# Kernel tuning notes

Measured on AMD Instinct MI355X. Metric: run time of the kernel, lower is better.

## Reference

```python
import jax, jax.numpy as jnp
import numpy as np

N_NODES = 50000


def _gine(x, src, dst, edge_embed, lin_w, lin_b, nn_w, nn_b):
    # PyG GINEConv (eps=0): out = nn(x + sum_{j->i} ReLU(x_j + lin(edge_attr)))
    e = edge_embed @ lin_w + lin_b              # [E, d_in]
    msg = jax.nn.relu(x[src] + e)               # gather + fuse, [E, d_in]
    agg = jax.ops.segment_sum(msg, dst, num_segments=N_NODES)  # scatter-add, [N, d_in]
    return (x + agg) @ nn_w + nn_b              # small MLP, [N, d_out]


def setup_inputs() -> dict:
    key = jax.random.key(0)
    ks = jax.random.split(key, 20)
    E = 800000
    h = 128
    sc = lambda f_in: 1.0 / np.sqrt(f_in)
    inp = {
        "x": jax.random.normal(ks[0], (N_NODES, 1), jnp.float32),
        "edge_index": jax.random.randint(ks[1], (2, E), 0, N_NODES, jnp.int64),
        "edge_attr": jax.random.normal(ks[2], (E, 1), jnp.float32),
        "em_w": jax.random.normal(ks[3], (1, h), jnp.float32) * sc(1),
        "em_b": jnp.zeros((h,), jnp.float32),
        "l1_w": jax.random.normal(ks[4], (h, 1), jnp.float32) * sc(h),
        "l1_b": jnp.zeros((1,), jnp.float32),
        "n1_w": jax.random.normal(ks[5], (1, h), jnp.float32) * sc(1),
        "n1_b": jnp.zeros((h,), jnp.float32),
        "l2_w": jax.random.normal(ks[6], (h, h), jnp.float32) * sc(h),
        "l2_b": jnp.zeros((h,), jnp.float32),
        "n2_w": jax.random.normal(ks[7], (h, h), jnp.float32) * sc(h),
        "n2_b": jnp.zeros((h,), jnp.float32),
        "l3_w": jax.random.normal(ks[8], (h, h), jnp.float32) * sc(h),
        "l3_b": jnp.zeros((h,), jnp.float32),
        "n3_w": jax.random.normal(ks[9], (h, h), jnp.float32) * sc(h),
        "n3_b": jnp.zeros((h,), jnp.float32),
        "dec_w": jax.random.normal(ks[10], (2 * h, 1), jnp.float32) * sc(2 * h),
        "dec_b": jnp.zeros((1,), jnp.float32),
    }
    return inp


def reference(x, edge_index, edge_attr, em_w, em_b, l1_w, l1_b, n1_w, n1_b,
              l2_w, l2_b, n2_w, n2_b, l3_w, l3_b, n3_w, n3_b, dec_w, dec_b):
    src, dst = edge_index[0], edge_index[1]
    edge_embed = edge_attr @ em_w + em_b                      # [E, 128]
    hdn = _gine(x,   src, dst, edge_embed, l1_w, l1_b, n1_w, n1_b)
    hdn = _gine(hdn, src, dst, edge_embed, l2_w, l2_b, n2_w, n2_b)
    hdn = _gine(hdn, src, dst, edge_embed, l3_w, l3_b, n3_w, n3_b)
    h_cat = jnp.concatenate([hdn[src], hdn[dst]], axis=-1)    # [E, 256]
    return h_cat @ dec_w + dec_b                              # [E, 1]
```

## Files before the change

kernel.cpp:

```cpp
#include <hip/hip_runtime.h>

#define H 128
#define CAPC 3072


typedef unsigned long long ull;
using bf16x8 = __attribute__((ext_vector_type(8))) short;
using f32x4  = __attribute__((ext_vector_type(4))) float;

__device__ __forceinline__ float bf2f(unsigned short v) {
  return __uint_as_float(((unsigned)v) << 16);
}
__device__ __forceinline__ unsigned short bf16r(float v) {
  unsigned u = __float_as_uint(v);
  u = (u + 0x7FFFu + ((u >> 16) & 1u)) >> 16;
  return (unsigned short)u;
}
__device__ __forceinline__ unsigned bf16pair(float a, float b) {
  return (unsigned)bf16r(a) | ((unsigned)bf16r(b) << 16);
}

__global__ __launch_bounds__(256) void init_consts(
    const float* __restrict__ em_w, const float* __restrict__ em_b,
    const float* __restrict__ l1_w, const float* __restrict__ l1_b,
    const float* __restrict__ l2_w, const float* __restrict__ l2_b,
    const float* __restrict__ n1_b,
    const float* __restrict__ l3_w, const float* __restrict__ l3_b,
    const float* __restrict__ n2w, const float* __restrict__ n3w,
    float* __restrict__ consts, int* __restrict__ cursor,
    unsigned short* __restrict__ w2t, unsigned short* __restrict__ w3t) {
  if (blockIdx.x > 0) {
    const int i = (blockIdx.x - 1) * 256 + threadIdx.x;
    if (i < H * H) {
      const int j = i >> 7, k = i & (H - 1);
      w2t[k * H + j] = bf16r(n2w[i]);
    } else {
      const int ii = i - H * H;
      const int j = ii >> 7, k = ii & (H - 1);
      w3t[k * H + j] = bf16r(n3w[ii]);
    }
    return;
  }
  const int k = threadIdx.x;
  cursor[k] = 0;
  cursor[k + 256] = 0;
  __shared__ float sa[H], sc[H];
  if (k < H) {
    float u2 = 0.f, c2 = 0.f, u3 = 0.f, c3 = 0.f;
    for (int j = 0; j < H; ++j) {
      const float ew = em_w[j], eb = em_b[j];
      u2 = fmaf(ew, l2_w[j * H + k], u2);
      c2 = fmaf(eb, l2_w[j * H + k], c2);
      u3 = fmaf(ew, l3_w[j * H + k], u3);
      c3 = fmaf(eb, l3_w[j * H + k], c3);
    }
    consts[2 + k]         = u2;
    consts[2 + H + k]     = c2 + l2_b[k] + n1_b[k];
    consts[2 + 2 * H + k] = u3;
    consts[2 + 3 * H + k] = c3 + l3_b[k];
    sa[k] = em_w[k] * l1_w[k];
    sc[k] = em_b[k] * l1_w[k];
  }
  __syncthreads();
  for (int s = 64; s > 0; s >>= 1) {
    if (k < s) { sa[k] += sa[k + s]; sc[k] += sc[k + s]; }
    __syncthreads();
  }
  if (k == 0) { consts[0] = sa[0]; consts[1] = sc[0] + l1_b[0]; }
}

__global__ __launch_bounds__(1024) void bin_scatter(
    const int* __restrict__ src, const int* __restrict__ dst,
    const float* __restrict__ ea, int* __restrict__ cursor,
    ull* __restrict__ spc, int E, int NBUCK) {
  __shared__ int lhist[512];
  __shared__ int lbase[512];
  const int tid = threadIdx.x;
  const int base = blockIdx.x * 2048 + tid * 2;
  if (tid < 512) lhist[tid] = 0;
  __syncthreads();
  int s_[2], d_[2], b_[2], r_[2];
  float a_[2];
#pragma unroll
  for (int j = 0; j < 2; ++j) {
    const int e = base + j;
    if (e < E) {
      s_[j] = src[e]; d_[j] = dst[e]; a_[j] = ea[e];
      b_[j] = d_[j] >> 7;
      r_[j] = atomicAdd(&lhist[b_[j]], 1);
    } else {
      b_[j] = -1;
    }
  }
  __syncthreads();
  if (tid < NBUCK && lhist[tid] > 0)
    lbase[tid] = atomicAdd(&cursor[tid], lhist[tid]);
  __syncthreads();
#pragma unroll
  for (int j = 0; j < 2; ++j) {
    if (b_[j] >= 0) {
      const int pl = lbase[b_[j]] + r_[j];
      if (pl < CAPC)
        spc[(size_t)b_[j] * CAPC + pl] =
            ((ull)(unsigned)(s_[j] | ((d_[j] & 127) << 16)) << 32) |
            (ull)(unsigned)__float_as_uint(a_[j]);
    }
  }
}

__global__ __launch_bounds__(1024) void fine_scatter(
    const int* __restrict__ cursor, const ull* __restrict__ spc,
    const float* __restrict__ x, const float* __restrict__ consts,
    int2* __restrict__ spf, int* __restrict__ rowstart,
    float* __restrict__ s1, int N) {
  __shared__ int lh[128];
  __shared__ int sd[128];
  __shared__ int cur[128];
  __shared__ int2 pay[CAPC];
  const int tid = threadIdx.x;
  const int b = blockIdx.x;
  const int cnt = min(cursor[b], CAPC);
  const size_t rbase = (size_t)b * CAPC;
  if (tid < 128) lh[tid] = 0;
  __syncthreads();
  for (int i = tid; i < cnt; i += 1024)
    atomicAdd(&lh[(int)((spc[rbase + i] >> 48) & 127u)], 1);
  __syncthreads();
  if (tid < 128) sd[tid] = lh[tid];
  __syncthreads();
  for (int off = 1; off < 128; off <<= 1) {
    int t = 0;
    if (tid < 128 && tid >= off) t = sd[tid - off];
    __syncthreads();
    if (tid < 128) sd[tid] += t;
    __syncthreads();
  }
  if (tid < 128) {
    const int ex = sd[tid] - lh[tid];
    cur[tid] = ex;
    rowstart[b * 129 + tid] = (int)rbase + ex;
    if (tid == 0) rowstart[b * 129 + 128] = (int)rbase + cnt;
  }
  __syncthreads();
  for (int i = tid; i < cnt; i += 1024) {
    const ull payv = spc[rbase + i];
    const int dl = (int)((payv >> 48) & 127u);
    const int pos = atomicAdd(&cur[dl], 1);
    pay[pos] = make_int2((int)((payv >> 32) & 0xFFFFu), (int)(unsigned)payv);
  }
  __syncthreads();
  for (int i = tid; i < cnt; i += 1024) spf[rbase + i] = pay[i];
  const int lane = tid & 63, w = tid >> 6;
  const float a1 = consts[0], c1 = consts[1];
  for (int i = w; i < 128; i += 16) {
    const int n = (b << 7) + i;
    if (n >= N) break;
    const int rsl = sd[i] - lh[i], ci = lh[i];
    float part = 0.f;
    for (int j = lane; j < ci; j += 64) {
      const int2 pv = pay[rsl + j];
      part += fmaxf(x[pv.x] + fmaf(a1, __int_as_float(pv.y), c1), 0.f);
    }
#pragma unroll
    for (int o = 32; o >= 1; o >>= 1) part += __shfl_xor(part, o, 64);
    if (lane == 0) s1[n] = x[n] + part;
  }
}

__global__ __launch_bounds__(1024) void layer2_fused(
    const int* __restrict__ rowstart, const int2* __restrict__ sp,
    const float* __restrict__ s1, const float* __restrict__ n1w,
    const float* __restrict__ n1b, const float* __restrict__ consts,
    const unsigned short* __restrict__ w2t, const float* __restrict__ n2b,
    unsigned short* __restrict__ h2b, int N) {
  __shared__ unsigned short t2s[16][136];
  __shared__ unsigned short hs[16][128];
  const int tid = threadIdx.x, w = tid >> 6, lane = tid & 63;
  const int node0 = blockIdx.x * 16;
  {
    const int n = node0 + w;
    if (n < N) {
      const int rb = (n >> 7) * 129 + (n & 127);
      const int rs = rowstart[rb], re = rowstart[rb + 1];
      const float w0 = n1w[lane],            w1 = n1w[lane + 64];
      const float u0 = consts[2 + lane],     u1 = consts[2 + lane + 64];
      const float c0 = consts[2 + H + lane], c1 = consts[2 + H + lane + 64];
      float acc0 = 0.f, acc1 = 0.f;
      for (int base = rs; base < re; base += 64) {
        const int i = base + lane;
        float s1v = 0.f, eav = 0.f;
        if (i < re) {
          const int2 sv = sp[i];
          s1v = s1[sv.x];
          eav = __int_as_float(sv.y);
        }
        const int cntv = min(64, re - base);
        for (int j = 0; j < cntv; ++j) {
          const float s = __shfl(s1v, j, 64);
          const float a = __shfl(eav, j, 64);
          acc0 += fmaxf(fmaf(s, w0, fmaf(a, u0, c0)), 0.f);
          acc1 += fmaxf(fmaf(s, w1, fmaf(a, u1, c1)), 0.f);
        }
      }
      const float sn = s1[n];
      t2s[w][lane]      = bf16r(fmaf(sn, w0, n1b[lane])      + acc0);
      t2s[w][lane + 64] = bf16r(fmaf(sn, w1, n1b[lane + 64]) + acc1);
    } else {
      t2s[w][lane] = 0;
      t2s[w][lane + 64] = 0;
    }
  }
  __syncthreads();
  if (w < 8) {
    const int t = w, col = lane & 15, quad = lane >> 4;
    const bf16x8 a0 = *(const bf16x8*)&t2s[col][quad * 8];
    const bf16x8 a1 = *(const bf16x8*)&t2s[col][32 + quad * 8];
    const bf16x8 a2 = *(const bf16x8*)&t2s[col][64 + quad * 8];
    const bf16x8 a3 = *(const bf16x8*)&t2s[col][96 + quad * 8];
    const bf16x8* bcol =
        (const bf16x8*)(w2t + (size_t)(t * 16 + col) * H + quad * 8);
    f32x4 acc = {0.f, 0.f, 0.f, 0.f};
    acc = __builtin_amdgcn_mfma_f32_16x16x32_bf16(a0, bcol[0], acc, 0, 0, 0);
    acc = __builtin_amdgcn_mfma_f32_16x16x32_bf16(a1, bcol[4], acc, 0, 0, 0);
    acc = __builtin_amdgcn_mfma_f32_16x16x32_bf16(a2, bcol[8], acc, 0, 0, 0);
    acc = __builtin_amdgcn_mfma_f32_16x16x32_bf16(a3, bcol[12], acc, 0, 0, 0);
    const float bias = n2b[t * 16 + col];
#pragma unroll
    for (int r = 0; r < 4; ++r)
      hs[quad * 4 + r][t * 16 + col] = bf16r(acc[r] + bias);
  }
  __syncthreads();
  const int row = tid >> 6, word = tid & 63;
  ((unsigned*)h2b)[(size_t)(node0 + row) * 64 + word] =
      ((const unsigned*)hs)[row * 64 + word];
}

__global__ __launch_bounds__(1024) void layer3_fused(
    const int* __restrict__ rowstart, const int2* __restrict__ sp,
    const unsigned short* __restrict__ h2b, const float* __restrict__ consts,
    const unsigned short* __restrict__ w3t, const float* __restrict__ n3b,
    const float* __restrict__ dec_w, float* __restrict__ p,
    float* __restrict__ q, int N) {
  __shared__ unsigned short t3s[16][136];
  __shared__ float ps[16], qs[16];
  const int tid = threadIdx.x, w = tid >> 6, lane = tid & 63;
  const int node0 = blockIdx.x * 16;
  if (tid < 16) { ps[tid] = 0.f; qs[tid] = 0.f; }
  {
    const int n = node0 + w;
    const int k0 = 2 * lane;
    if (n < N) {
      const int rb = (n >> 7) * 129 + (n & 127);
      const int rs = rowstart[rb], re = rowstart[rb + 1];
      const float u0 = consts[2 + 2 * H + k0], u1 = consts[2 + 2 * H + k0 + 1];
      const float c0 = consts[2 + 3 * H + k0], c1 = consts[2 + 3 * H + k0 + 1];
      float acc0 = 0.f, acc1 = 0.f;
      for (int base = rs; base < re; base += 64) {
        const int i = base + lane;
        int esrc = 0;
        float eav = 0.f;
        if (i < re) {
          const int2 sv = sp[i];
          esrc = sv.x;
          eav = __int_as_float(sv.y);
        }
        const int cntv = min(64, re - base);
        int j = 0;
        for (; j + 4 <= cntv; j += 4) {
          const int s0 = __shfl(esrc, j, 64),     s1i = __shfl(esrc, j + 1, 64);
          const int s2 = __shfl(esrc, j + 2, 64), s3 = __shfl(esrc, j + 3, 64);
          const float a0 = __shfl(eav, j, 64),     a1 = __shfl(eav, j + 1, 64);
          const float a2 = __shfl(eav, j + 2, 64), a3 = __shfl(eav, j + 3, 64);
          const ushort2 h0 = *(const ushort2*)&h2b[(size_t)s0 * H + k0];
          const ushort2 h1 = *(const ushort2*)&h2b[(size_t)s1i * H + k0];
          const ushort2 h2v = *(const ushort2*)&h2b[(size_t)s2 * H + k0];
          const ushort2 h3 = *(const ushort2*)&h2b[(size_t)s3 * H + k0];
          acc0 += fmaxf(bf2f(h0.x) + fmaf(a0, u0, c0), 0.f);
          acc1 += fmaxf(bf2f(h0.y) + fmaf(a0, u1, c1), 0.f);
          acc0 += fmaxf(bf2f(h1.x) + fmaf(a1, u0, c0), 0.f);
          acc1 += fmaxf(bf2f(h1.y) + fmaf(a1, u1, c1), 0.f);
          acc0 += fmaxf(bf2f(h2v.x) + fmaf(a2, u0, c0), 0.f);
          acc1 += fmaxf(bf2f(h2v.y) + fmaf(a2, u1, c1), 0.f);
          acc0 += fmaxf(bf2f(h3.x) + fmaf(a3, u0, c0), 0.f);
          acc1 += fmaxf(bf2f(h3.y) + fmaf(a3, u1, c1), 0.f);
        }
        for (; j < cntv; ++j) {
          const int s0 = __shfl(esrc, j, 64);
          const float a0 = __shfl(eav, j, 64);
          const ushort2 hv = *(const ushort2*)&h2b[(size_t)s0 * H + k0];
          acc0 += fmaxf(bf2f(hv.x) + fmaf(a0, u0, c0), 0.f);
          acc1 += fmaxf(bf2f(hv.y) + fmaf(a0, u1, c1), 0.f);
        }
      }
      const ushort2 hn = *(const ushort2*)&h2b[(size_t)n * H + k0];
      *(unsigned*)&t3s[w][k0] = bf16pair(bf2f(hn.x) + acc0, bf2f(hn.y) + acc1);
    } else {
      *(unsigned*)&t3s[w][k0] = 0u;
    }
  }
  __syncthreads();
  if (w < 8) {
    const int t = w, col = lane & 15, quad = lane >> 4;
    const bf16x8 a0 = *(const bf16x8*)&t3s[col][quad * 8];
    const bf16x8 a1 = *(const bf16x8*)&t3s[col][32 + quad * 8];
    const bf16x8 a2 = *(const bf16x8*)&t3s[col][64 + quad * 8];
    const bf16x8 a3 = *(const bf16x8*)&t3s[col][96 + quad * 8];
    const bf16x8* bcol =
        (const bf16x8*)(w3t + (size_t)(t * 16 + col) * H + quad * 8);
    f32x4 acc = {0.f, 0.f, 0.f, 0.f};
    acc = __builtin_amdgcn_mfma_f32_16x16x32_bf16(a0, bcol[0], acc, 0, 0, 0);
    acc = __builtin_amdgcn_mfma_f32_16x16x32_bf16(a1, bcol[4], acc, 0, 0, 0);
    acc = __builtin_amdgcn_mfma_f32_16x16x32_bf16(a2, bcol[8], acc, 0, 0, 0);
    acc = __builtin_amdgcn_mfma_f32_16x16x32_bf16(a3, bcol[12], acc, 0, 0, 0);
    const float bias = n3b[t * 16 + col];
    const float dA = dec_w[t * 16 + col];
    const float dB = dec_w[128 + t * 16 + col];
    float pP[4], qP[4];
#pragma unroll
    for (int r = 0; r < 4; ++r) {
      const float h = acc[r] + bias;
      pP[r] = h * dA;
      qP[r] = h * dB;
    }
#pragma unroll
    for (int o = 1; o < 16; o <<= 1) {
#pragma unroll
      for (int r = 0; r < 4; ++r) {
        pP[r] += __shfl_xor(pP[r], o, 64);
        qP[r] += __shfl_xor(qP[r], o, 64);
      }
    }
    if (col == 0) {
#pragma unroll
      for (int r = 0; r < 4; ++r) {
        atomicAdd(&ps[quad * 4 + r], pP[r]);
        atomicAdd(&qs[quad * 4 + r], qP[r]);
      }
    }
  }
  __syncthreads();
  if (tid < 16) {
    const int n = node0 + tid;
    if (n < N) { p[n] = ps[tid]; q[n] = qs[tid]; }
  }
}

__global__ void final_kernel(const int* __restrict__ src,
                             const int* __restrict__ dst,
                             const float* __restrict__ p,
                             const float* __restrict__ q,
                             const float* __restrict__ dec_b,
                             float* __restrict__ out, int E) {
  const int e = blockIdx.x * blockDim.x + threadIdx.x;
  if (e < E) out[e] = p[src[e]] + q[dst[e]] + dec_b[0];
}

extern "C" void kernel_launch(void* const* d_in, const int* in_sizes, int n_in,
                              void* d_out, int out_size, void* d_ws, size_t ws_size,
                              hipStream_t stream) {
  const float* x     = (const float*)d_in[0];
  const int*   ei    = (const int*)d_in[1];
  const float* ea    = (const float*)d_in[2];
  const float* em_w  = (const float*)d_in[3];
  const float* em_b  = (const float*)d_in[4];
  const float* l1_w  = (const float*)d_in[5];
  const float* l1_b  = (const float*)d_in[6];
  const float* n1_w  = (const float*)d_in[7];
  const float* n1_b  = (const float*)d_in[8];
  const float* l2_w  = (const float*)d_in[9];
  const float* l2_b  = (const float*)d_in[10];
  const float* n2_w  = (const float*)d_in[11];
  const float* n2_b  = (const float*)d_in[12];
  const float* l3_w  = (const float*)d_in[13];
  const float* l3_b  = (const float*)d_in[14];
  const float* n3_w  = (const float*)d_in[15];
  const float* n3_b  = (const float*)d_in[16];
  const float* dec_w = (const float*)d_in[17];
  const float* dec_b = (const float*)d_in[18];
  float* out = (float*)d_out;

  const int N = in_sizes[0];
  const int E = in_sizes[2];
  const int* src = ei;
  const int* dst = ei + E;

  const int NBUCK  = (N + 127) >> 7;
  const int NBATCH = (E + 2047) >> 11;
  const int NPAD   = ((N + 15) / 16) * 16;
  const int NT16   = NPAD / 16;

  float* ws       = (float*)d_ws;
  float* consts   = ws;
  ull*   spc      = (ull*)(ws + 1024);
  int2*  spf      = (int2*)(spc + (size_t)NBUCK * CAPC);
  unsigned short* h2b = (unsigned short*)(spf + (size_t)NBUCK * CAPC);
  unsigned short* w2t = h2b + (size_t)NPAD * H;
  unsigned short* w3t = w2t + H * H;
  float* s1       = (float*)(w3t + H * H);
  float* p        = s1 + N;
  float* q        = p + N;
  int*   cursor   = (int*)(q + N);
  int*   rowstart = cursor + 512;

  init_consts<<<129, 256, 0, stream>>>(em_w, em_b, l1_w, l1_b, l2_w, l2_b,
                                       n1_b, l3_w, l3_b, n2_w, n3_w,
                                       consts, cursor, w2t, w3t);
  bin_scatter<<<NBATCH, 1024, 0, stream>>>(src, dst, ea, cursor, spc, E, NBUCK);
  fine_scatter<<<NBUCK, 1024, 0, stream>>>(cursor, spc, x, consts, spf,
                                           rowstart, s1, N);
  layer2_fused<<<NT16, 1024, 0, stream>>>(rowstart, spf, s1, n1_w, n1_b,
                                          consts, w2t, n2_b, h2b, N);
  layer3_fused<<<NT16, 1024, 0, stream>>>(rowstart, spf, h2b, consts, w3t,
                                          n3_b, dec_w, p, q, N);
  final_kernel<<<(E + 255) / 256, 256, 0, stream>>>(src, dst, p, q, dec_b, out, E);
}
```

Before: 230.9 us.

## Fold layer-3 MLP into decoder vectors, replacing MFMA with per-node dot products

Because layer 3's output feeds only the linear decoder, the change precomputes n3_w·dec_w halves (vA, vB) and the bias terms in init_consts. Layer 3 then reduces each node's aggregated feature vector to two scalars p and q with a wave dot product. This drops the MFMA GEMM, the shared-memory staging, the block syncs and the w3t transpose. Layer 3 now runs as 256-thread blocks with one wave per node. Numerics change slightly because the aggregate stays in fp32 instead of being rounded to bf16 before the GEMM.

Result: faster. 219.4 us (median of 2 runs) (-5.0%).

```diff
diff --git a/kernel.cpp b/kernel.cpp
--- a/kernel.cpp
+++ b/kernel.cpp
@@ -27,17 +27,14 @@
     const float* __restrict__ n1_b,
     const float* __restrict__ l3_w, const float* __restrict__ l3_b,
     const float* __restrict__ n2w, const float* __restrict__ n3w,
+    const float* __restrict__ n3b, const float* __restrict__ dec_w,
     float* __restrict__ consts, int* __restrict__ cursor,
-    unsigned short* __restrict__ w2t, unsigned short* __restrict__ w3t) {
+    unsigned short* __restrict__ w2t) {
   if (blockIdx.x > 0) {
     const int i = (blockIdx.x - 1) * 256 + threadIdx.x;
     if (i < H * H) {
       const int j = i >> 7, k = i & (H - 1);
       w2t[k * H + j] = bf16r(n2w[i]);
-    } else {
-      const int ii = i - H * H;
-      const int j = ii >> 7, k = ii & (H - 1);
-      w3t[k * H + j] = bf16r(n3w[ii]);
     }
     return;
   }
@@ -46,18 +43,22 @@
   cursor[k + 256] = 0;
   __shared__ float sa[H], sc[H];
   if (k < H) {
-    float u2 = 0.f, c2 = 0.f, u3 = 0.f, c3 = 0.f;
+    float u2 = 0.f, c2 = 0.f, u3 = 0.f, c3 = 0.f, vA = 0.f, vB = 0.f;
     for (int j = 0; j < H; ++j) {
       const float ew = em_w[j], eb = em_b[j];
       u2 = fmaf(ew, l2_w[j * H + k], u2);
       c2 = fmaf(eb, l2_w[j * H + k], c2);
       u3 = fmaf(ew, l3_w[j * H + k], u3);
       c3 = fmaf(eb, l3_w[j * H + k], c3);
+      vA = fmaf(n3w[k * H + j], dec_w[j], vA);
+      vB = fmaf(n3w[k * H + j], dec_w[H + j], vB);
     }
     consts[2 + k]         = u2;
     consts[2 + H + k]     = c2 + l2_b[k] + n1_b[k];
     consts[2 + 2 * H + k] = u3;
     consts[2 + 3 * H + k] = c3 + l3_b[k];
+    consts[514 + k]       = vA;
+    consts[642 + k]       = vB;
     sa[k] = em_w[k] * l1_w[k];
     sc[k] = em_b[k] * l1_w[k];
   }
@@ -67,6 +68,17 @@
     __syncthreads();
   }
   if (k == 0) { consts[0] = sa[0]; consts[1] = sc[0] + l1_b[0]; }
+  __syncthreads();
+  if (k < H) {
+    sa[k] = n3b[k] * dec_w[k];
+    sc[k] = n3b[k] * dec_w[H + k];
+  }
+  __syncthreads();
+  for (int s = 64; s > 0; s >>= 1) {
+    if (k < s) { sa[k] += sa[k + s]; sc[k] += sc[k + s]; }
+    __syncthreads();
+  }
+  if (k == 0) { consts[770] = sa[0]; consts[771] = sc[0]; }
 }
 
 __global__ __launch_bounds__(1024) void bin_scatter(
@@ -235,113 +247,71 @@
       ((const unsigned*)hs)[row * 64 + word];
 }
 
-__global__ __launch_bounds__(1024) void layer3_fused(
+__global__ __launch_bounds__(256) void layer3_dot(
     const int* __restrict__ rowstart, const int2* __restrict__ sp,
     const unsigned short* __restrict__ h2b, const float* __restrict__ consts,
-    const unsigned short* __restrict__ w3t, const float* __restrict__ n3b,
-    const float* __restrict__ dec_w, float* __restrict__ p,
-    float* __restrict__ q, int N) {
-  __shared__ unsigned short t3s[16][136];
-  __shared__ float ps[16], qs[16];
-  const int tid = threadIdx.x, w = tid >> 6, lane = tid & 63;
-  const int node0 = blockIdx.x * 16;
-  if (tid < 16) { ps[tid] = 0.f; qs[tid] = 0.f; }
-  {
-    const int n = node0 + w;
-    const int k0 = 2 * lane;
-    if (n < N) {
-      const int rb = (n >> 7) * 129 + (n & 127);
-      const int rs = rowstart[rb], re = rowstart[rb + 1];
-      const float u0 = consts[2 + 2 * H + k0], u1 = consts[2 + 2 * H + k0 + 1];
-      const float c0 = consts[2 + 3 * H + k0], c1 = consts[2 + 3 * H + k0 + 1];
-      float acc0 = 0.f, acc1 = 0.f;
-      for (int base = rs; base < re; base += 64) {
-        const int i = base + lane;
-        int esrc = 0;
-        float eav = 0.f;
-        if (i < re) {
-          const int2 sv = sp[i];
-          esrc = sv.x;
-          eav = __int_as_float(sv.y);
-        }
-        const int cntv = min(64, re - base);
-        int j = 0;
-        for (; j + 4 <= cntv; j += 4) {
-          const int s0 = __shfl(esrc, j, 64),     s1i = __shfl(esrc, j + 1, 64);
-          const int s2 = __shfl(esrc, j + 2, 64), s3 = __shfl(esrc, j + 3, 64);
-          const float a0 = __shfl(eav, j, 64),     a1 = __shfl(eav, j + 1, 64);
-          const float a2 = __shfl(eav, j + 2, 64), a3 = __shfl(eav, j + 3, 64);
-          const ushort2 h0 = *(const ushort2*)&h2b[(size_t)s0 * H + k0];
-          const ushort2 h1 = *(const ushort2*)&h2b[(size_t)s1i * H + k0];
-          const ushort2 h2v = *(const ushort2*)&h2b[(size_t)s2 * H + k0];
-          const ushort2 h3 = *(const ushort2*)&h2b[(size_t)s3 * H + k0];
-          acc0 += fmaxf(bf2f(h0.x) + fmaf(a0, u0, c0), 0.f);
-          acc1 += fmaxf(bf2f(h0.y) + fmaf(a0, u1, c1), 0.f);
-          acc0 += fmaxf(bf2f(h1.x) + fmaf(a1, u0, c0), 0.f);
-          acc1 += fmaxf(bf2f(h1.y) + fmaf(a1, u1, c1), 0.f);
-          acc0 += fmaxf(bf2f(h2v.x) + fmaf(a2, u0, c0), 0.f);
-          acc1 += fmaxf(bf2f(h2v.y) + fmaf(a2, u1, c1), 0.f);
-          acc0 += fmaxf(bf2f(h3.x) + fmaf(a3, u0, c0), 0.f);
-          acc1 += fmaxf(bf2f(h3.y) + fmaf(a3, u1, c1), 0.f);
-        }
-        for (; j < cntv; ++j) {
-          const int s0 = __shfl(esrc, j, 64);
-          const float a0 = __shfl(eav, j, 64);
-          const ushort2 hv = *(const ushort2*)&h2b[(size_t)s0 * H + k0];
-          acc0 += fmaxf(bf2f(hv.x) + fmaf(a0, u0, c0), 0.f);
-          acc1 += fmaxf(bf2f(hv.y) + fmaf(a0, u1, c1), 0.f);
-        }
-      }
-      const ushort2 hn = *(const ushort2*)&h2b[(size_t)n * H + k0];
-      *(unsigned*)&t3s[w][k0] = bf16pair(bf2f(hn.x) + acc0, bf2f(hn.y) + acc1);
-    } else {
-      *(unsigned*)&t3s[w][k0] = 0u;
-    }
-  }
-  __syncthreads();
-  if (w < 8) {
-    const int t = w, col = lane & 15, quad = lane >> 4;
-    const bf16x8 a0 = *(const bf16x8*)&t3s[col][quad * 8];
-    const bf16x8 a1 = *(const bf16x8*)&t3s[col][32 + quad * 8];
-    const bf16x8 a2 = *(const bf16x8*)&t3s[col][64 + quad * 8];
-    const bf16x8 a3 = *(const bf16x8*)&t3s[col][96 + quad * 8];
-    const bf16x8* bcol =
-        (const bf16x8*)(w3t + (size_t)(t * 16 + col) * H + quad * 8);
-    f32x4 acc = {0.f, 0.f, 0.f, 0.f};
-    acc = __builtin_amdgcn_mfma_f32_16x16x32_bf16(a0, bcol[0], acc, 0, 0, 0);
-    acc = __builtin_amdgcn_mfma_f32_16x16x32_bf16(a1, bcol[4], acc, 0, 0, 0);
-    acc = __builtin_amdgcn_mfma_f32_16x16x32_bf16(a2, bcol[8], acc, 0, 0, 0);
-    acc = __builtin_amdgcn_mfma_f32_16x16x32_bf16(a3, bcol[12], acc, 0, 0, 0);
-    const float bias = n3b[t * 16 + col];
-    const float dA = dec_w[t * 16 + col];
-    const float dB = dec_w[128 + t * 16 + col];
-    float pP[4], qP[4];
-#pragma unroll
-    for (int r = 0; r < 4; ++r) {
-      const float h = acc[r] + bias;
-      pP[r] = h * dA;
-      qP[r] = h * dB;
-    }
-#pragma unroll
-    for (int o = 1; o < 16; o <<= 1) {
-#pragma unroll
-      for (int r = 0; r < 4; ++r) {
-        pP[r] += __shfl_xor(pP[r], o, 64);
-        qP[r] += __shfl_xor(qP[r], o, 64);
-      }
-    }
-    if (col == 0) {
-#pragma unroll
-      for (int r = 0; r < 4; ++r) {
-        atomicAdd(&ps[quad * 4 + r], pP[r]);
-        atomicAdd(&qs[quad * 4 + r], qP[r]);
-      }
-    }
-  }
-  __syncthreads();
-  if (tid < 16) {
-    const int n = node0 + tid;
-    if (n < N) { p[n] = ps[tid]; q[n] = qs[tid]; }
+    float* __restrict__ p, float* __restrict__ q, int N) {
+  const int n = (blockIdx.x * blockDim.x + threadIdx.x) >> 6;
+  const int lane = threadIdx.x & 63;
+  if (n >= N) return;
+  const int k0 = 2 * lane;
+  const float u0 = consts[2 + 2 * H + k0], u1 = consts[2 + 2 * H + k0 + 1];
+  const float c0 = consts[2 + 3 * H + k0], c1 = consts[2 + 3 * H + k0 + 1];
+  const float vA0 = consts[514 + k0], vA1 = consts[514 + k0 + 1];
+  const float vB0 = consts[642 + k0], vB1 = consts[642 + k0 + 1];
+  const int rb = (n >> 7) * 129 + (n & 127);
+  const int rs = rowstart[rb], re = rowstart[rb + 1];
+  float acc0 = 0.f, acc1 = 0.f;
+  for (int base = rs; base < re; base += 64) {
+    const int i = base + lane;
+    int esrc = 0;
+    float eav = 0.f;
+    if (i < re) {
+      const int2 sv = sp[i];
+      esrc = sv.x;
+      eav = __int_as_float(sv.y);
+    }
+    const int cntv = min(64, re - base);
+    int j = 0;
+    for (; j + 4 <= cntv; j += 4) {
+      const int s0 = __shfl(esrc, j, 64),     s1i = __shfl(esrc, j + 1, 64);
+      const int s2 = __shfl(esrc, j + 2, 64), s3 = __shfl(esrc, j + 3, 64);
+      const float a0 = __shfl(eav, j, 64),     a1 = __shfl(eav, j + 1, 64);
+      const float a2 = __shfl(eav, j + 2, 64), a3 = __shfl(eav, j + 3, 64);
+      const ushort2 h0 = *(const ushort2*)&h2b[(size_t)s0 * H + k0];
+      const ushort2 h1 = *(const ushort2*)&h2b[(size_t)s1i * H + k0];
+      const ushort2 h2v = *(const ushort2*)&h2b[(size_t)s2 * H + k0];
+      const ushort2 h3 = *(const ushort2*)&h2b[(size_t)s3 * H + k0];
+      acc0 += fmaxf(bf2f(h0.x) + fmaf(a0, u0, c0), 0.f);
+      acc1 += fmaxf(bf2f(h0.y) + fmaf(a0, u1, c1), 0.f);
+      acc0 += fmaxf(bf2f(h1.x) + fmaf(a1, u0, c0), 0.f);
+      acc1 += fmaxf(bf2f(h1.y) + fmaf(a1, u1, c1), 0.f);
+      acc0 += fmaxf(bf2f(h2v.x) + fmaf(a2, u0, c0), 0.f);
+      acc1 += fmaxf(bf2f(h2v.y) + fmaf(a2, u1, c1), 0.f);
+      acc0 += fmaxf(bf2f(h3.x) + fmaf(a3, u0, c0), 0.f);
+      acc1 += fmaxf(bf2f(h3.y) + fmaf(a3, u1, c1), 0.f);
+    }
+    for (; j < cntv; ++j) {
+      const int s0 = __shfl(esrc, j, 64);
+      const float a0 = __shfl(eav, j, 64);
+      const ushort2 hv = *(const ushort2*)&h2b[(size_t)s0 * H + k0];
+      acc0 += fmaxf(bf2f(hv.x) + fmaf(a0, u0, c0), 0.f);
+      acc1 += fmaxf(bf2f(hv.y) + fmaf(a0, u1, c1), 0.f);
+    }
+  }
+  const ushort2 hn = *(const ushort2*)&h2b[(size_t)n * H + k0];
+  const float t0 = bf2f(hn.x) + acc0;
+  const float t1 = bf2f(hn.y) + acc1;
+  float pd = t0 * vA0 + t1 * vA1;
+  float qd = t0 * vB0 + t1 * vB1;
+#pragma unroll
+  for (int o = 32; o >= 1; o >>= 1) {
+    pd += __shfl_xor(pd, o, 64);
+    qd += __shfl_xor(qd, o, 64);
+  }
+  if (lane == 0) {
+    p[n] = pd + consts[770];
+    q[n] = qd + consts[771];
   }
 }
 
@@ -395,22 +365,21 @@
   int2*  spf      = (int2*)(spc + (size_t)NBUCK * CAPC);
   unsigned short* h2b = (unsigned short*)(spf + (size_t)NBUCK * CAPC);
   unsigned short* w2t = h2b + (size_t)NPAD * H;
-  unsigned short* w3t = w2t + H * H;
-  float* s1       = (float*)(w3t + H * H);
+  float* s1       = (float*)(w2t + H * H);
   float* p        = s1 + N;
   float* q        = p + N;
   int*   cursor   = (int*)(q + N);
   int*   rowstart = cursor + 512;
 
-  init_consts<<<129, 256, 0, stream>>>(em_w, em_b, l1_w, l1_b, l2_w, l2_b,
-                                       n1_b, l3_w, l3_b, n2_w, n3_w,
-                                       consts, cursor, w2t, w3t);
+  init_consts<<<65, 256, 0, stream>>>(em_w, em_b, l1_w, l1_b, l2_w, l2_b,
+                                      n1_b, l3_w, l3_b, n2_w, n3_w, n3_b,
+                                      dec_w, consts, cursor, w2t);
   bin_scatter<<<NBATCH, 1024, 0, stream>>>(src, dst, ea, cursor, spc, E, NBUCK);
   fine_scatter<<<NBUCK, 1024, 0, stream>>>(cursor, spc, x, consts, spf,
                                            rowstart, s1, N);
   layer2_fused<<<NT16, 1024, 0, stream>>>(rowstart, spf, s1, n1_w, n1_b,
                                           consts, w2t, n2_b, h2b, N);
-  layer3_fused<<<NT16, 1024, 0, stream>>>(rowstart, spf, h2b, consts, w3t,
-                                          n3_b, dec_w, p, q, N);
+  layer3_dot<<<(N + 3) / 4, 256, 0, stream>>>(rowstart, spf, h2b, consts,
+                                              p, q, N);
   final_kernel<<<(E + 255) / 256, 256, 0, stream>>>(src, dst, p, q, dec_b, out, E);
 }
```
